# Kernel tuning notes

Hardware: AMD Instinct MI355X
Metric: run time of the kernel (lower is better)

The kernel has to match this reference:

```python
import jax, jax.numpy as jnp
import numpy as np

N_NODES = 100000
N_EDGES = 800000
N_LABEL = 262144
IN, H, OUT = 16, 256, 128
BN_EPS = 1e-5


def setup_inputs() -> dict:
    key = jax.random.key(0)
    ks = jax.random.split(key, 32)
    def lin(k, fi, fo):
        return jax.random.normal(k, (fi, fo), jnp.float32) / np.sqrt(fi)
    inp = {
        "x": jax.random.normal(ks[0], (N_NODES, IN), jnp.float32),
        "edge_index": jax.random.randint(ks[1], (2, N_EDGES), 0, N_NODES, jnp.int32),
        "edge_weight": jax.random.uniform(ks[2], (N_EDGES,), jnp.float32),
        "edge_label_index": jax.random.randint(ks[3], (2, N_LABEL), 0, N_NODES, jnp.int32),
        # encoder GCN layers: 4 convs, BN on first 3
        "W1": lin(ks[4], IN, H),  "b1": jnp.zeros((H,), jnp.float32),
        "g1": jnp.ones((H,), jnp.float32), "be1": jnp.zeros((H,), jnp.float32),
        "W2": lin(ks[5], H, H),   "b2": jnp.zeros((H,), jnp.float32),
        "g2": jnp.ones((H,), jnp.float32), "be2": jnp.zeros((H,), jnp.float32),
        "W3": lin(ks[6], H, H),   "b3": jnp.zeros((H,), jnp.float32),
        "g3": jnp.ones((H,), jnp.float32), "be3": jnp.zeros((H,), jnp.float32),
        "W4": lin(ks[7], H, OUT), "b4": jnp.zeros((OUT,), jnp.float32),
        # decoder MLP on concatenated pair embeddings
        "D1W": lin(ks[8], 2 * OUT, OUT), "D1b": jnp.zeros((OUT,), jnp.float32),
        "D2W": lin(ks[9], OUT, OUT),     "D2b": jnp.zeros((OUT,), jnp.float32),
        "D3W": lin(ks[10], OUT, 1),      "D3b": jnp.zeros((1,), jnp.float32),
    }
    return inp


def _forward(x, edge_index, edge_weight, edge_label_index,
             W1, b1, g1, be1, W2, b2, g2, be2, W3, b3, g3, be3, W4, b4,
             D1W, D1b, D2W, D2b, D3W, D3b):
    n = x.shape[0]
    src, dst = edge_index[0], edge_index[1]
    # GCN symmetric normalization with self-loops (weight 1)
    deg = jax.ops.segment_sum(edge_weight, dst, num_segments=n) + 1.0
    dinv = jax.lax.rsqrt(deg)
    edge_norm = dinv[src] * edge_weight * dinv[dst]   # [E]
    self_norm = dinv * dinv                            # [N]

    def gcn(h, W, b):
        h = h @ W                                      # [N, F]
        agg = jax.ops.segment_sum(h[src] * edge_norm[:, None], dst, num_segments=n)
        return agg + h * self_norm[:, None] + b

    def bn(h, g, be):  # training-mode BatchNorm1d over node dim
        m = h.mean(axis=0)
        v = h.var(axis=0)
        return (h - m) * jax.lax.rsqrt(v + BN_EPS) * g + be

    h = jax.nn.relu(bn(gcn(x, W1, b1), g1, be1))
    h = jax.nn.relu(bn(gcn(h, W2, b2), g2, be2))
    h = jax.nn.relu(bn(gcn(h, W3, b3), g3, be3))
    z = gcn(h, W4, b4)                                 # [N, OUT] encoded

    # decode: gather both endpoints, concat, MLP + sigmoid
    e0, e1 = edge_label_index[0], edge_label_index[1]
    q = jnp.concatenate([z[e0], z[e1]], axis=1)        # [EL, 2*OUT]
    q = jax.nn.relu(q @ D1W + D1b)
    q = jax.nn.relu(q @ D2W + D2b)
    p = jax.nn.sigmoid(q @ D3W + D3b)
    return p.squeeze(-1)                               # [EL]


def reference(x, edge_index, edge_weight, edge_label_index,
              W1, b1, g1, be1, W2, b2, g2, be2, W3, b3, g3, be3, W4, b4,
              D1W, D1b, D2W, D2b, D3W, D3b):
    return _forward(x, edge_index, edge_weight, edge_label_index,
                    W1, b1, g1, be1, W2, b2, g2, be2, W3, b3, g3, be3, W4, b4,
                    D1W, D1b, D2W, D2b, D3W, D3b)
```

## Files before the change

### kernel.cpp

```cpp
#include <hip/hip_runtime.h>
#include <cmath>

#define NN 100000
#define NE 800000
#define NL 262144
#define GB 782

typedef __attribute__((ext_vector_type(8))) short bf16x8;
typedef __attribute__((ext_vector_type(4))) float f32x4;

__device__ __forceinline__ unsigned short f2bf(float f) {
  unsigned int u = __builtin_bit_cast(unsigned int, f);
  u = (u + 0x7FFF + ((u >> 16) & 1)) >> 16;
  return (unsigned short)u;
}
__device__ __forceinline__ float bf2f(unsigned short u) {
  return __builtin_bit_cast(float, (unsigned int)u << 16);
}

__global__ void k_degcnt(const int* __restrict__ dst, const float* __restrict__ w,
                         unsigned long long* __restrict__ dc) {
  int e = blockIdx.x * 256 + threadIdx.x;
  if (e < NE) {
    unsigned long long pk = (1ULL << 32) | (unsigned long long)(unsigned int)(w[e] * 8388608.0f);
    atomicAdd(&dc[dst[e]], pk);
  }
}
__global__ void k_dinv2(const unsigned long long* __restrict__ dc,
                        float* __restrict__ dinv, int* __restrict__ cnt) {
  int n = blockIdx.x * 256 + threadIdx.x;
  if (n < NN) {
    unsigned long long v = dc[n];
    cnt[n] = (int)(v >> 32);
    dinv[n] = rsqrtf((float)(unsigned int)v * (1.0f / 8388608.0f) + 1.0f);
  }
}
__global__ void k_scan1(const int* __restrict__ cnt, int* __restrict__ tsum) {
  __shared__ int s[256];
  int t = threadIdx.x;
  int base = blockIdx.x * 1024;
  int acc = 0;
  for (int i = 0; i < 4; i++) { int idx = base + t * 4 + i; if (idx < NN) acc += cnt[idx]; }
  s[t] = acc; __syncthreads();
  for (int o = 128; o > 0; o >>= 1) { if (t < o) s[t] += s[t + o]; __syncthreads(); }
  if (t == 0) tsum[blockIdx.x] = s[0];
}
__global__ void k_scan2(const int* __restrict__ tsum, int* __restrict__ toff, int nt, int* __restrict__ rowptr_end) {
  __shared__ int s[256];
  int t = threadIdx.x;
  int v = (t < nt) ? tsum[t] : 0;
  s[t] = v; __syncthreads();
  for (int o = 1; o < 256; o <<= 1) { int xv = (t >= o) ? s[t - o] : 0; __syncthreads(); s[t] += xv; __syncthreads(); }
  if (t < nt) toff[t] = s[t] - v;
  if (t == 255) *rowptr_end = s[255];
}
__global__ void k_scan3(const int* __restrict__ cnt, const int* __restrict__ toff,
                        int* __restrict__ rowptr, int* __restrict__ nxt) {
  __shared__ int s[256];
  int t = threadIdx.x;
  int base = blockIdx.x * 1024 + t * 4;
  int v[4]; int tot = 0;
  for (int i = 0; i < 4; i++) { int idx = base + i; v[i] = (idx < NN) ? cnt[idx] : 0; tot += v[i]; }
  s[t] = tot; __syncthreads();
  for (int o = 1; o < 256; o <<= 1) { int xv = (t >= o) ? s[t - o] : 0; __syncthreads(); s[t] += xv; __syncthreads(); }
  int excl = s[t] - tot + toff[blockIdx.x];
  for (int i = 0; i < 4; i++) {
    int idx = base + i;
    if (idx < NN) { rowptr[idx] = excl; nxt[idx] = excl; }
    excl += v[i];
  }
}
__global__ void k_scatter2(const int* __restrict__ src, const int* __restrict__ dst, const float* __restrict__ w,
                           const float* __restrict__ dinv, int* __restrict__ nxt,
                           int* __restrict__ esp, float* __restrict__ enp) {
  int e = blockIdx.x * 256 + threadIdx.x;
  if (e < NE) {
    int d = dst[e], s = src[e];
    int p = atomicAdd(&nxt[d], 1);
    esp[p] = s; enp[p] = dinv[s] * w[e] * dinv[d];
  }
}

__global__ void k_cvt_wT(const float* __restrict__ W, unsigned short* __restrict__ Wt, int K, int N) {
  int id = blockIdx.x * 256 + threadIdx.x;
  if (id >= K * N) return;
  int n = id / K, k = id - n * K;
  Wt[id] = f2bf(W[k * N + n]);
}

__global__ void k_pack(const unsigned short* __restrict__ Wt, unsigned short* __restrict__ P, int K, int NJ) {
  int id = blockIdx.x * 256 + threadIdx.x;
  int total = (K / 32) * NJ * 64;
  if (id >= total) return;
  int lane = id & 63, g = id >> 6;
  int j = g % NJ, s = g / NJ;
  int fr = lane & 15, fq = lane >> 4;
  uint4 v = *(const uint4*)(Wt + (size_t)(j * 16 + fr) * K + s * 32 + fq * 8);
  *(uint4*)(P + (size_t)id * 8) = v;
}

__global__ __launch_bounds__(256) void k_wuv(const float* __restrict__ W4, const float* __restrict__ D1W,
                                             const float* __restrict__ b4, const float* __restrict__ D1b,
                                             unsigned short* __restrict__ wtUV, float* __restrict__ buv) {
  __shared__ float dc[256];
  int j = blockIdx.x;
  int k = threadIdx.x;
  dc[k] = D1W[k * 128 + j];
  __syncthreads();
  float su = 0.f, sv = 0.f;
  const float* w4r = W4 + k * 128;
  for (int p = 0; p < 128; p++) { float w = w4r[p]; su += w * dc[p]; sv += w * dc[128 + p]; }
  wtUV[(size_t)j * 256 + k] = f2bf(su);
  wtUV[(size_t)(128 + j) * 256 + k] = f2bf(sv);
  if (k == 0) {
    float bu = D1b[j], bv = 0.f;
    for (int p = 0; p < 128; p++) { bu += b4[p] * dc[p]; bv += b4[p] * dc[128 + p]; }
    buv[j] = bu; buv[128 + j] = bv;
  }
}

__global__ __launch_bounds__(256) void k_gemm16(const float* __restrict__ x, const float* __restrict__ W,
                                                unsigned short* __restrict__ out) {
  __shared__ float xs[32][16];
  int t = threadIdx.x; int row0 = blockIdx.x * 32;
  for (int i = t; i < 512; i += 256) {
    int r = i >> 4, c = i & 15; int row = row0 + r;
    xs[r][c] = (row < NN) ? x[(size_t)row * 16 + c] : 0.f;
  }
  float w[16];
  #pragma unroll
  for (int k = 0; k < 16; k++) w[k] = W[k * 256 + t];
  __syncthreads();
  for (int r = 0; r < 32; r++) {
    int row = row0 + r; if (row >= NN) break;
    float acc = 0.f;
    #pragma unroll
    for (int k = 0; k < 16; k++) acc += xs[r][k] * w[k];
    out[(size_t)row * 256 + t] = f2bf(acc);
  }
}

template <bool STATS>
__global__ __launch_bounds__(512) void k_gemm_v12(
    const unsigned short* __restrict__ A, const unsigned short* __restrict__ Wp,
    const float* __restrict__ bias, unsigned short* __restrict__ C,
    float* __restrict__ Ps, float* __restrict__ Pq) {
  __shared__ unsigned short S[128 * 264];
  const int t = threadIdx.x;
  const int lane = t & 63, w = t >> 6, fr = lane & 15, fq = lane >> 4;
  const int row0 = blockIdx.x * 128;
  bf16x8 B0[8], B1[8];
  #pragma unroll
  for (int s = 0; s < 8; s++) {
    B0[s] = *(const bf16x8*)(Wp + ((size_t)(s * 16 + 2 * w) * 64 + lane) * 8);
    B1[s] = *(const bf16x8*)(Wp + ((size_t)(s * 16 + 2 * w + 1) * 64 + lane) * 8);
  }
  {
    int r = t >> 2, q = t & 3;
    int row = row0 + r;
    uint4* dst = (uint4*)(S + r * 264 + q * 64);
    if (row < NN) {
      const uint4* src = (const uint4*)(A + (size_t)row * 256 + q * 64);
      #pragma unroll
      for (int i = 0; i < 8; i++) dst[i] = src[i];
    } else {
      #pragma unroll
      for (int i = 0; i < 8; i++) dst[i] = make_uint4(0, 0, 0, 0);
    }
  }
  __syncthreads();
  f32x4 acc[8][2] = {};
  #pragma unroll
  for (int r = 0; r < 8; r++) {
    #pragma unroll
    for (int s = 0; s < 8; s++) {
      bf16x8 a = *(const bf16x8*)(S + (r * 16 + fr) * 264 + s * 32 + fq * 8);
      acc[r][0] = __builtin_amdgcn_mfma_f32_16x16x32_bf16(a, B0[s], acc[r][0], 0, 0, 0);
      acc[r][1] = __builtin_amdgcn_mfma_f32_16x16x32_bf16(a, B1[s], acc[r][1], 0, 0, 0);
    }
  }
  #pragma unroll
  for (int jl = 0; jl < 2; jl++) {
    const int col = w * 32 + jl * 16 + fr;
    float bj = bias[col];
    float s_ = 0.f, q_ = 0.f;
    #pragma unroll
    for (int r = 0; r < 8; r++) {
      #pragma unroll
      for (int rr = 0; rr < 4; rr++) {
        int row = row0 + r * 16 + fq * 4 + rr;
        if (row < NN) {
          float c = acc[r][jl][rr] + bj;
          C[(size_t)row * 256 + col] = f2bf(c);
          if (STATS) { s_ += c; q_ += c * c; }
        }
      }
    }
    if (STATS) {
      s_ += __shfl_xor(s_, 16); q_ += __shfl_xor(q_, 16);
      s_ += __shfl_xor(s_, 32); q_ += __shfl_xor(q_, 32);
      if (fq == 0) {
        Ps[(size_t)blockIdx.x * 256 + col] = s_;
        Pq[(size_t)blockIdx.x * 256 + col] = q_;
      }
    }
  }
}

__global__ __launch_bounds__(256) void k_bnred(const float* __restrict__ Ps, const float* __restrict__ Pq,
                                               const float* __restrict__ g, const float* __restrict__ be,
                                               float* __restrict__ scale, float* __restrict__ shift) {
  __shared__ float Ss[256], Sq[256];
  const int f = blockIdx.x;
  const int t = threadIdx.x;
  float s = 0.f, q = 0.f;
  for (int p = t; p < GB; p += 256) { s += Ps[(size_t)p * 256 + f]; q += Pq[(size_t)p * 256 + f]; }
  Ss[t] = s; Sq[t] = q;
  __syncthreads();
  for (int o = 128; o > 0; o >>= 1) { if (t < o) { Ss[t] += Ss[t + o]; Sq[t] += Sq[t + o]; } __syncthreads(); }
  if (t == 0) {
    float m = Ss[0] * (1.f / NN);
    float v = Sq[0] * (1.f / NN) - m * m;
    float sc = g[f] * rsqrtf(v + 1e-5f);
    scale[f] = sc; shift[f] = be[f] - m * sc;
  }
}

__device__ __forceinline__ void ld8(const unsigned short* p, float* f) {
  uint4 v = *(const uint4*)p;
  unsigned int u[4] = {v.x, v.y, v.z, v.w};
  #pragma unroll
  for (int i = 0; i < 4; i++) {
    f[2 * i] = bf2f((unsigned short)(u[i] & 0xFFFF));
    f[2 * i + 1] = bf2f((unsigned short)(u[i] >> 16));
  }
}
template <bool BN>
__global__ __launch_bounds__(256) void k_agg5(const unsigned short* __restrict__ hb,
    const int* __restrict__ esp, const float* __restrict__ enp,
    const int* __restrict__ rowptr, const float* __restrict__ dinv,
    const float* __restrict__ scale, const float* __restrict__ shift,
    const float* __restrict__ bias, unsigned short* __restrict__ outb) {
  const int lane = threadIdx.x & 63;
  const int lg = lane & 31;
  const int srcbase = lane & 32;
  const int n = blockIdx.x * 8 + (threadIdx.x >> 5);
  const int f0 = lg * 8;
  float sc8[8] = {}, sh8[8] = {};
  if constexpr (BN) {
    #pragma unroll
    for (int j = 0; j < 8; j++) { sc8[j] = scale[f0 + j]; sh8[j] = shift[f0 + j]; }
  }
  auto xf = [&](float v, int j) -> float {
    if constexpr (BN) return fmaxf(v * sc8[j] + sh8[j], 0.f);
    else return v;
  };
  float d = dinv[n]; float dd = d * d;
  float acc[8];
  {
    float sv[8];
    ld8(hb + (size_t)n * 256 + f0, sv);
    #pragma unroll
    for (int j = 0; j < 8; j++) acc[j] = xf(sv[j], j) * dd + (BN ? 0.f : bias[f0 + j]);
  }
  const int i0 = rowptr[n];
  const int dg = rowptr[n + 1] - i0;
  int sreg = 0; float wreg = 0.f;
  if (lg < dg) { sreg = esp[i0 + lg]; wreg = enp[i0 + lg]; }
  const int m = (dg < 32) ? dg : 32;
  int e = 0;
  for (; e + 4 <= m; e += 4) {
    int s0 = __shfl(sreg, srcbase | e), s1 = __shfl(sreg, srcbase | (e + 1));
    int s2 = __shfl(sreg, srcbase | (e + 2)), s3 = __shfl(sreg, srcbase | (e + 3));
    float w0 = __shfl(wreg, srcbase | e), w1 = __shfl(wreg, srcbase | (e + 1));
    float w2 = __shfl(wreg, srcbase | (e + 2)), w3 = __shfl(wreg, srcbase | (e + 3));
    float r0[8], r1[8], r2[8], r3[8];
    ld8(hb + (size_t)s0 * 256 + f0, r0);
    ld8(hb + (size_t)s1 * 256 + f0, r1);
    ld8(hb + (size_t)s2 * 256 + f0, r2);
    ld8(hb + (size_t)s3 * 256 + f0, r3);
    #pragma unroll
    for (int j = 0; j < 8; j++)
      acc[j] += w0 * xf(r0[j], j) + w1 * xf(r1[j], j) + w2 * xf(r2[j], j) + w3 * xf(r3[j], j);
  }
  for (; e < m; e++) {
    int s0 = __shfl(sreg, srcbase | e); float w0 = __shfl(wreg, srcbase | e);
    float r0[8];
    ld8(hb + (size_t)s0 * 256 + f0, r0);
    #pragma unroll
    for (int j = 0; j < 8; j++) acc[j] += w0 * xf(r0[j], j);
  }
  for (int i = i0 + 32; i < i0 + dg; i++) {
    int s0 = esp[i]; float w0 = enp[i];
    float r0[8];
    ld8(hb + (size_t)s0 * 256 + f0, r0);
    #pragma unroll
    for (int j = 0; j < 8; j++) acc[j] += w0 * xf(r0[j], j);
  }
  unsigned int o[4];
  #pragma unroll
  for (int i = 0; i < 4; i++)
    o[i] = (unsigned int)f2bf(acc[2 * i]) | ((unsigned int)f2bf(acc[2 * i + 1]) << 16);
  *(uint4*)(outb + (size_t)n * 256 + f0) = make_uint4(o[0], o[1], o[2], o[3]);
}

__global__ __launch_bounds__(256) void k_bnstats2(const unsigned short* __restrict__ h,
                                                  float* __restrict__ sums, float* __restrict__ sqs) {
  __shared__ float L[4][256];
  int t = threadIdx.x;
  int fp = t & 127;
  size_t rbase = (size_t)blockIdx.x * 256 + (t >> 7);
  float s0 = 0, q0 = 0, s1 = 0, q1 = 0;
  for (int i = 0; i < 128; i++) {
    size_t r = rbase + 2 * (size_t)i;
    if (r >= NN) break;
    unsigned int v = *(const unsigned int*)&h[r * 256 + fp * 2];
    float a = bf2f((unsigned short)(v & 0xFFFF));
    float b = bf2f((unsigned short)(v >> 16));
    s0 += a; q0 += a * a; s1 += b; q1 += b * b;
  }
  L[0][t] = s0; L[1][t] = q0; L[2][t] = s1; L[3][t] = q1;
  __syncthreads();
  if (t < 128) {
    s0 = L[0][t] + L[0][t + 128]; q0 = L[1][t] + L[1][t + 128];
    s1 = L[2][t] + L[2][t + 128]; q1 = L[3][t] + L[3][t + 128];
    atomicAdd(&sums[2 * t], s0); atomicAdd(&sqs[2 * t], q0);
    atomicAdd(&sums[2 * t + 1], s1); atomicAdd(&sqs[2 * t + 1], q1);
  }
}
__global__ void k_bnfinal(const float* __restrict__ sums, const float* __restrict__ sqs,
                          const float* __restrict__ g, const float* __restrict__ be,
                          float* __restrict__ scale, float* __restrict__ shift) {
  int f = threadIdx.x;
  float m = sums[f] * (1.f / NN);
  float v = sqs[f] * (1.f / NN) - m * m;
  float sc = g[f] * rsqrtf(v + 1e-5f);
  scale[f] = sc; shift[f] = be[f] - m * sc;
}

__global__ __launch_bounds__(256) void k_decoder3(
    const unsigned short* __restrict__ uv,
    const int* __restrict__ l0, const int* __restrict__ l1,
    const unsigned short* __restrict__ W2p, const float* __restrict__ D2b,
    const float* __restrict__ D3W, const float* __restrict__ D3b,
    float* __restrict__ out) {
  __shared__ unsigned short S[128 * 136];
  __shared__ int ei0[128], ei1[128];
  const int t = threadIdx.x;
  const int base = blockIdx.x * 128;
  if (t < 128) ei0[t] = l0[base + t];
  else ei1[t - 128] = l1[base + t - 128];
  __syncthreads();
  {
    int e = t >> 1, h = t & 1;
    const uint4* pu = (const uint4*)(uv + (size_t)ei0[e] * 256 + h * 64);
    const uint4* pv = (const uint4*)(uv + (size_t)ei1[e] * 256 + 128 + h * 64);
    uint4* dst = (uint4*)(S + e * 136 + h * 64);
    #pragma unroll
    for (int i = 0; i < 8; i++) {
      uint4 a = pu[i], b = pv[i];
      unsigned int ia[4] = {a.x, a.y, a.z, a.w};
      unsigned int ib[4] = {b.x, b.y, b.z, b.w};
      unsigned int o[4];
      #pragma unroll
      for (int p = 0; p < 4; p++) {
        float lo = fmaxf(bf2f((unsigned short)(ia[p] & 0xFFFF)) + bf2f((unsigned short)(ib[p] & 0xFFFF)), 0.f);
        float hi = fmaxf(bf2f((unsigned short)(ia[p] >> 16)) + bf2f((unsigned short)(ib[p] >> 16)), 0.f);
        o[p] = (unsigned int)f2bf(lo) | ((unsigned int)f2bf(hi) << 16);
      }
      dst[i] = make_uint4(o[0], o[1], o[2], o[3]);
    }
  }
  __syncthreads();
  const int lane = t & 63, w = t >> 6, fr = lane & 15, fq = lane >> 4;
  f32x4 acc2[2][8] = {};
  #pragma unroll
  for (int s = 0; s < 4; s++) {
    bf16x8 a0 = *(const bf16x8*)(S + (w * 32 + fr) * 136 + s * 32 + fq * 8);
    bf16x8 a1 = *(const bf16x8*)(S + (w * 32 + 16 + fr) * 136 + s * 32 + fq * 8);
    #pragma unroll
    for (int j = 0; j < 8; j++) {
      bf16x8 bw = *(const bf16x8*)(W2p + ((size_t)(s * 8 + j) * 64 + lane) * 8);
      acc2[0][j] = __builtin_amdgcn_mfma_f32_16x16x32_bf16(a0, bw, acc2[0][j], 0, 0, 0);
      acc2[1][j] = __builtin_amdgcn_mfma_f32_16x16x32_bf16(a1, bw, acc2[1][j], 0, 0, 0);
    }
  }
  float b2v[8], w3v[8];
  #pragma unroll
  for (int j = 0; j < 8; j++) { b2v[j] = D2b[j * 16 + fr]; w3v[j] = D3W[j * 16 + fr]; }
  float d3b = D3b[0];
  #pragma unroll
  for (int f = 0; f < 2; f++) {
    float p[4] = {0.f, 0.f, 0.f, 0.f};
    #pragma unroll
    for (int j = 0; j < 8; j++)
      #pragma unroll
      for (int r = 0; r < 4; r++)
        p[r] += fmaxf(acc2[f][j][r] + b2v[j], 0.f) * w3v[j];
    #pragma unroll
    for (int r = 0; r < 4; r++) {
      p[r] += __shfl_xor(p[r], 1);
      p[r] += __shfl_xor(p[r], 2);
      p[r] += __shfl_xor(p[r], 4);
      p[r] += __shfl_xor(p[r], 8);
      if (fr == 0) out[base + w * 32 + f * 16 + fq * 4 + r] = 1.f / (1.f + expf(-(p[r] + d3b)));
    }
  }
}

extern "C" void kernel_launch(void* const* d_in, const int* in_sizes, int n_in,
                              void* d_out, int out_size, void* d_ws, size_t ws_size,
                              hipStream_t stream) {
  const float* x = (const float*)d_in[0];
  const int* ei = (const int*)d_in[1];
  const int* esrc = ei; const int* edst = ei + NE;
  const float* ew = (const float*)d_in[2];
  const int* eli = (const int*)d_in[3];
  const int* l0 = eli; const int* l1 = eli + NL;
  const float* W1 = (const float*)d_in[4],  *b1 = (const float*)d_in[5];
  const float* g1 = (const float*)d_in[6],  *be1 = (const float*)d_in[7];
  const float* W2 = (const float*)d_in[8],  *b2 = (const float*)d_in[9];
  const float* g2 = (const float*)d_in[10], *be2 = (const float*)d_in[11];
  const float* W3 = (const float*)d_in[12], *b3 = (const float*)d_in[13];
  const float* g3 = (const float*)d_in[14], *be3 = (const float*)d_in[15];
  const float* W4 = (const float*)d_in[16], *b4 = (const float*)d_in[17];
  const float* D1W = (const float*)d_in[18], *D1b = (const float*)d_in[19];
  const float* D2W = (const float*)d_in[20], *D2b = (const float*)d_in[21];
  const float* D3W = (const float*)d_in[22], *D3b = (const float*)d_in[23];
  float* out = (float*)d_out;

  float* wf = (float*)d_ws;
  size_t off = 0;
  auto A = [&](size_t n) { float* p = wf + off; off += (n + 63) & ~(size_t)63; return p; };
  float* dinv = A(NN);
  float* enp = A(NE);
  float* sums = A(256);
  float* sqs = A(256);
  float* scale = A(256);
  float* shift = A(256);
  float* buv = A(256);
  float* Ps = A((size_t)GB * 256);
  float* Pq = A((size_t)GB * 256);
  unsigned long long* dc = (unsigned long long*)A(2 * (size_t)NN);
  int* cnt = (int*)A(NN);
  int* rowptr = (int*)A(NN + 1);
  int* nxt = (int*)A(NN);
  int* esp = (int*)A(NE);
  int* tsum = (int*)A(256);
  int* toff = (int*)A(256);
  unsigned short* hbA = (unsigned short*)A((size_t)NN * 128);
  unsigned short* hbB = (unsigned short*)A((size_t)NN * 128);
  unsigned short* uv  = (unsigned short*)A((size_t)NN * 128);
  unsigned short* wt2 = (unsigned short*)A(256 * 128);
  unsigned short* wt3 = (unsigned short*)A(256 * 128);
  unsigned short* wtUV = (unsigned short*)A(256 * 128);
  unsigned short* w2t = (unsigned short*)A(64 * 128);
  unsigned short* wp2 = (unsigned short*)A(256 * 128);
  unsigned short* wp3 = (unsigned short*)A(256 * 128);
  unsigned short* wpUV = (unsigned short*)A(256 * 128);
  unsigned short* w2p = (unsigned short*)A(64 * 128);

  const int EB = (NE + 255) / 256;
  const int NB = (NN + 255) / 256;
  const int ST = (NN + 1023) / 1024;
  const int AB = NN / 8;

  hipMemsetAsync(dc, 0, (size_t)NN * 8, stream);
  k_degcnt<<<EB, 256, 0, stream>>>(edst, ew, dc);
  k_dinv2<<<NB, 256, 0, stream>>>(dc, dinv, cnt);
  k_scan1<<<ST, 256, 0, stream>>>(cnt, tsum);
  k_scan2<<<1, 256, 0, stream>>>(tsum, toff, ST, rowptr + NN);
  k_scan3<<<ST, 256, 0, stream>>>(cnt, toff, rowptr, nxt);
  k_scatter2<<<EB, 256, 0, stream>>>(esrc, edst, ew, dinv, nxt, esp, enp);

  k_cvt_wT<<<(256 * 256 + 255) / 256, 256, 0, stream>>>(W2, wt2, 256, 256);
  k_cvt_wT<<<(256 * 256 + 255) / 256, 256, 0, stream>>>(W3, wt3, 256, 256);
  k_cvt_wT<<<(128 * 128 + 255) / 256, 256, 0, stream>>>(D2W, w2t, 128, 128);
  k_wuv<<<128, 256, 0, stream>>>(W4, D1W, b4, D1b, wtUV, buv);
  k_pack<<<32, 256, 0, stream>>>(wt2, wp2, 256, 16);
  k_pack<<<32, 256, 0, stream>>>(wt3, wp3, 256, 16);
  k_pack<<<32, 256, 0, stream>>>(wtUV, wpUV, 256, 16);
  k_pack<<<8, 256, 0, stream>>>(w2t, w2p, 128, 8);

  k_gemm16<<<(NN + 31) / 32, 256, 0, stream>>>(x, W1, hbA);
  k_agg5<false><<<AB, 256, 0, stream>>>(hbA, esp, enp, rowptr, dinv, nullptr, nullptr, b1, hbB);
  hipMemsetAsync(sums, 0, 512 * sizeof(float), stream);
  k_bnstats2<<<NB, 256, 0, stream>>>(hbB, sums, sqs);
  k_bnfinal<<<1, 256, 0, stream>>>(sums, sqs, g1, be1, scale, shift);

  k_agg5<true><<<AB, 256, 0, stream>>>(hbB, esp, enp, rowptr, dinv, scale, shift, nullptr, hbA);
  k_gemm_v12<true><<<GB, 512, 0, stream>>>(hbA, wp2, b2, hbB, Ps, Pq);
  k_bnred<<<256, 256, 0, stream>>>(Ps, Pq, g2, be2, scale, shift);

  k_agg5<true><<<AB, 256, 0, stream>>>(hbB, esp, enp, rowptr, dinv, scale, shift, nullptr, hbA);
  k_gemm_v12<true><<<GB, 512, 0, stream>>>(hbA, wp3, b3, hbB, Ps, Pq);
  k_bnred<<<256, 256, 0, stream>>>(Ps, Pq, g3, be3, scale, shift);

  k_agg5<true><<<AB, 256, 0, stream>>>(hbB, esp, enp, rowptr, dinv, scale, shift, nullptr, hbA);
  k_gemm_v12<false><<<GB, 512, 0, stream>>>(hbA, wpUV, buv, uv, nullptr, nullptr);

  k_decoder3<<<NL / 128, 256, 0, stream>>>(uv, l0, l1, w2p, D2b, D3W, D3b, out);
}
```

Baseline: 708.5 us.

## Reorder aggregation and matmul to aggregate on narrow feature widths

Layer 1 now aggregates the raw 16-wide input features before the 16x256 matmul. BN statistics are computed in the GEMM epilogue, which replaces the separate stats and final kernels. Layer 4 now applies BN+ReLU while loading the GEMM input, multiplies by W4 to 128 columns, aggregates at width 128, and then applies D1 as a separate 128->256 GEMM, instead of the folded W4·D1 256-wide product aggregated at 256. The goal is to cut gather traffic in the edge aggregations at the cost of one extra GEMM pass and an extra intermediate write and read in layer 4.

Result: faster. 606.9 us (-14.3%).

```diff
diff --git a/kernel.cpp b/kernel.cpp
--- a/kernel.cpp
+++ b/kernel.cpp
@@ -5,6 +5,7 @@
 #define NE 800000
 #define NL 262144
 #define GB 782
+#define NP1 3125
 
 typedef __attribute__((ext_vector_type(8))) short bf16x8;
 typedef __attribute__((ext_vector_type(4))) float f32x4;
@@ -87,6 +88,17 @@
   int n = id / K, k = id - n * K;
   Wt[id] = f2bf(W[k * N + n]);
 }
+__global__ void k_cvt_d1(const float* __restrict__ D1W, unsigned short* __restrict__ Wt) {
+  int id = blockIdx.x * 256 + threadIdx.x;
+  if (id >= 256 * 128) return;
+  int n = id >> 7, k = id & 127;
+  float v = (n < 128) ? D1W[(size_t)k * 128 + n] : D1W[(size_t)(128 + k) * 128 + (n - 128)];
+  Wt[id] = f2bf(v);
+}
+__global__ void k_biasuv(const float* __restrict__ D1b, float* __restrict__ buv) {
+  int t = threadIdx.x;
+  buv[t] = (t < 128) ? D1b[t] : 0.f;
+}
 
 __global__ void k_pack(const unsigned short* __restrict__ Wt, unsigned short* __restrict__ P, int K, int NJ) {
   int id = blockIdx.x * 256 + threadIdx.x;
@@ -99,89 +111,152 @@
   *(uint4*)(P + (size_t)id * 8) = v;
 }
 
-__global__ __launch_bounds__(256) void k_wuv(const float* __restrict__ W4, const float* __restrict__ D1W,
-                                             const float* __restrict__ b4, const float* __restrict__ D1b,
-                                             unsigned short* __restrict__ wtUV, float* __restrict__ buv) {
-  __shared__ float dc[256];
-  int j = blockIdx.x;
-  int k = threadIdx.x;
-  dc[k] = D1W[k * 128 + j];
-  __syncthreads();
-  float su = 0.f, sv = 0.f;
-  const float* w4r = W4 + k * 128;
-  for (int p = 0; p < 128; p++) { float w = w4r[p]; su += w * dc[p]; sv += w * dc[128 + p]; }
-  wtUV[(size_t)j * 256 + k] = f2bf(su);
-  wtUV[(size_t)(128 + j) * 256 + k] = f2bf(sv);
-  if (k == 0) {
-    float bu = D1b[j], bv = 0.f;
-    for (int p = 0; p < 128; p++) { bu += b4[p] * dc[p]; bv += b4[p] * dc[128 + p]; }
-    buv[j] = bu; buv[128 + j] = bv;
-  }
-}
-
-__global__ __launch_bounds__(256) void k_gemm16(const float* __restrict__ x, const float* __restrict__ W,
-                                                unsigned short* __restrict__ out) {
-  __shared__ float xs[32][16];
+__global__ __launch_bounds__(256) void k_agg16(const float* __restrict__ x,
+    const int* __restrict__ esp, const float* __restrict__ enp,
+    const int* __restrict__ rowptr, const float* __restrict__ dinv,
+    float* __restrict__ ax) {
+  const int t = threadIdx.x;
+  const int lane = t & 63;
+  const int g = lane >> 2, gl = lane & 3;
+  const int n = blockIdx.x * 64 + (t >> 6) * 16 + g;
+  if (n >= NN) return;
+  const float4* x4 = (const float4*)x;
+  float d = dinv[n]; float dd = d * d;
+  float4 self = x4[(size_t)n * 4 + gl];
+  float4 acc = make_float4(self.x * dd, self.y * dd, self.z * dd, self.w * dd);
+  const int i0 = rowptr[n];
+  const int dg = rowptr[n + 1] - i0;
+  int sreg[4]; float wreg[4];
+  #pragma unroll
+  for (int k = 0; k < 4; k++) {
+    int idx = gl + 4 * k;
+    if (idx < dg) { sreg[k] = esp[i0 + idx]; wreg[k] = enp[i0 + idx]; }
+    else { sreg[k] = 0; wreg[k] = 0.f; }
+  }
+  const int gbase = lane & ~3;
+  const int m4 = ((dg < 16 ? dg : 16) + 3) & ~3;
+  #pragma unroll 4
+  for (int e = 0; e < m4; e += 4) {
+    int k = e >> 2;
+    int s0, s1, s2, s3; float w0, w1, w2, w3;
+    switch (k) {
+      case 0: s0=__shfl(sreg[0],gbase|0); s1=__shfl(sreg[0],gbase|1); s2=__shfl(sreg[0],gbase|2); s3=__shfl(sreg[0],gbase|3);
+              w0=__shfl(wreg[0],gbase|0); w1=__shfl(wreg[0],gbase|1); w2=__shfl(wreg[0],gbase|2); w3=__shfl(wreg[0],gbase|3); break;
+      case 1: s0=__shfl(sreg[1],gbase|0); s1=__shfl(sreg[1],gbase|1); s2=__shfl(sreg[1],gbase|2); s3=__shfl(sreg[1],gbase|3);
+              w0=__shfl(wreg[1],gbase|0); w1=__shfl(wreg[1],gbase|1); w2=__shfl(wreg[1],gbase|2); w3=__shfl(wreg[1],gbase|3); break;
+      case 2: s0=__shfl(sreg[2],gbase|0); s1=__shfl(sreg[2],gbase|1); s2=__shfl(sreg[2],gbase|2); s3=__shfl(sreg[2],gbase|3);
+              w0=__shfl(wreg[2],gbase|0); w1=__shfl(wreg[2],gbase|1); w2=__shfl(wreg[2],gbase|2); w3=__shfl(wreg[2],gbase|3); break;
+      default: s0=__shfl(sreg[3],gbase|0); s1=__shfl(sreg[3],gbase|1); s2=__shfl(sreg[3],gbase|2); s3=__shfl(sreg[3],gbase|3);
+              w0=__shfl(wreg[3],gbase|0); w1=__shfl(wreg[3],gbase|1); w2=__shfl(wreg[3],gbase|2); w3=__shfl(wreg[3],gbase|3); break;
+    }
+    float4 r0 = x4[(size_t)s0 * 4 + gl], r1 = x4[(size_t)s1 * 4 + gl];
+    float4 r2 = x4[(size_t)s2 * 4 + gl], r3 = x4[(size_t)s3 * 4 + gl];
+    acc.x += w0 * r0.x + w1 * r1.x + w2 * r2.x + w3 * r3.x;
+    acc.y += w0 * r0.y + w1 * r1.y + w2 * r2.y + w3 * r3.y;
+    acc.z += w0 * r0.z + w1 * r1.z + w2 * r2.z + w3 * r3.z;
+    acc.w += w0 * r0.w + w1 * r1.w + w2 * r2.w + w3 * r3.w;
+  }
+  for (int i = i0 + 16; i < i0 + dg; i++) {
+    int s0 = esp[i]; float w0 = enp[i];
+    float4 r0 = x4[(size_t)s0 * 4 + gl];
+    acc.x += w0 * r0.x; acc.y += w0 * r0.y; acc.z += w0 * r0.z; acc.w += w0 * r0.w;
+  }
+  ((float4*)ax)[(size_t)n * 4 + gl] = acc;
+}
+
+__global__ __launch_bounds__(256) void k_gemm16s(const float* __restrict__ ax, const float* __restrict__ W,
+                                                 const float* __restrict__ b, unsigned short* __restrict__ out,
+                                                 float* __restrict__ Ps, float* __restrict__ Pq) {
+  __shared__ float xs[32][17];
   int t = threadIdx.x; int row0 = blockIdx.x * 32;
   for (int i = t; i < 512; i += 256) {
     int r = i >> 4, c = i & 15; int row = row0 + r;
-    xs[r][c] = (row < NN) ? x[(size_t)row * 16 + c] : 0.f;
+    xs[r][c] = (row < NN) ? ax[(size_t)row * 16 + c] : 0.f;
   }
   float w[16];
   #pragma unroll
   for (int k = 0; k < 16; k++) w[k] = W[k * 256 + t];
+  float bt = b[t];
   __syncthreads();
+  float s_ = 0.f, q_ = 0.f;
   for (int r = 0; r < 32; r++) {
     int row = row0 + r; if (row >= NN) break;
-    float acc = 0.f;
+    float acc = bt;
     #pragma unroll
     for (int k = 0; k < 16; k++) acc += xs[r][k] * w[k];
     out[(size_t)row * 256 + t] = f2bf(acc);
-  }
-}
-
-template <bool STATS>
+    s_ += acc; q_ += acc * acc;
+  }
+  Ps[(size_t)blockIdx.x * 256 + t] = s_;
+  Pq[(size_t)blockIdx.x * 256 + t] = q_;
+}
+
+template <int KDIM, int NCOLS, bool STATS, bool BNA>
 __global__ __launch_bounds__(512) void k_gemm_v12(
     const unsigned short* __restrict__ A, const unsigned short* __restrict__ Wp,
-    const float* __restrict__ bias, unsigned short* __restrict__ C,
-    float* __restrict__ Ps, float* __restrict__ Pq) {
-  __shared__ unsigned short S[128 * 264];
+    const float* __restrict__ bias, const float* __restrict__ bnsc, const float* __restrict__ bnsh,
+    unsigned short* __restrict__ C, float* __restrict__ Ps, float* __restrict__ Pq) {
+  constexpr int CPW = NCOLS / 128;
+  constexpr int KS = KDIM / 32;
+  constexpr int LDA = KDIM + 8;
+  constexpr int NU4 = KDIM / 32;
+  __shared__ unsigned short S[128 * LDA];
+  __shared__ float sc[BNA ? KDIM : 1], sh[BNA ? KDIM : 1];
   const int t = threadIdx.x;
   const int lane = t & 63, w = t >> 6, fr = lane & 15, fq = lane >> 4;
   const int row0 = blockIdx.x * 128;
-  bf16x8 B0[8], B1[8];
-  #pragma unroll
-  for (int s = 0; s < 8; s++) {
-    B0[s] = *(const bf16x8*)(Wp + ((size_t)(s * 16 + 2 * w) * 64 + lane) * 8);
-    B1[s] = *(const bf16x8*)(Wp + ((size_t)(s * 16 + 2 * w + 1) * 64 + lane) * 8);
-  }
+  if (BNA) {
+    if (t < KDIM) { sc[t] = bnsc[t]; sh[t] = bnsh[t]; }
+    __syncthreads();
+  }
+  bf16x8 B[CPW][KS];
+  #pragma unroll
+  for (int c = 0; c < CPW; c++)
+    #pragma unroll
+    for (int s = 0; s < KS; s++)
+      B[c][s] = *(const bf16x8*)(Wp + ((size_t)(s * (NCOLS / 16) + (w * CPW + c)) * 64 + lane) * 8);
   {
     int r = t >> 2, q = t & 3;
     int row = row0 + r;
-    uint4* dst = (uint4*)(S + r * 264 + q * 64);
+    uint4* dst = (uint4*)(S + r * LDA + q * (KDIM / 4));
     if (row < NN) {
-      const uint4* src = (const uint4*)(A + (size_t)row * 256 + q * 64);
+      const uint4* src = (const uint4*)(A + (size_t)row * KDIM + q * (KDIM / 4));
       #pragma unroll
-      for (int i = 0; i < 8; i++) dst[i] = src[i];
+      for (int i = 0; i < NU4; i++) {
+        uint4 v = src[i];
+        if (BNA) {
+          unsigned int u[4] = {v.x, v.y, v.z, v.w};
+          #pragma unroll
+          for (int p = 0; p < 4; p++) {
+            int colb = q * (KDIM / 4) + i * 8 + p * 2;
+            float lo = fmaxf(bf2f((unsigned short)(u[p] & 0xFFFF)) * sc[colb] + sh[colb], 0.f);
+            float hi = fmaxf(bf2f((unsigned short)(u[p] >> 16)) * sc[colb + 1] + sh[colb + 1], 0.f);
+            u[p] = (unsigned int)f2bf(lo) | ((unsigned int)f2bf(hi) << 16);
+          }
+          v = make_uint4(u[0], u[1], u[2], u[3]);
+        }
+        dst[i] = v;
+      }
     } else {
       #pragma unroll
-      for (int i = 0; i < 8; i++) dst[i] = make_uint4(0, 0, 0, 0);
+      for (int i = 0; i < NU4; i++) dst[i] = make_uint4(0, 0, 0, 0);
     }
   }
   __syncthreads();
-  f32x4 acc[8][2] = {};
+  f32x4 acc[8][CPW] = {};
   #pragma unroll
   for (int r = 0; r < 8; r++) {
     #pragma unroll
-    for (int s = 0; s < 8; s++) {
-      bf16x8 a = *(const bf16x8*)(S + (r * 16 + fr) * 264 + s * 32 + fq * 8);
-      acc[r][0] = __builtin_amdgcn_mfma_f32_16x16x32_bf16(a, B0[s], acc[r][0], 0, 0, 0);
-      acc[r][1] = __builtin_amdgcn_mfma_f32_16x16x32_bf16(a, B1[s], acc[r][1], 0, 0, 0);
-    }
-  }
-  #pragma unroll
-  for (int jl = 0; jl < 2; jl++) {
-    const int col = w * 32 + jl * 16 + fr;
+    for (int s = 0; s < KS; s++) {
+      bf16x8 a = *(const bf16x8*)(S + (r * 16 + fr) * LDA + s * 32 + fq * 8);
+      #pragma unroll
+      for (int c = 0; c < CPW; c++)
+        acc[r][c] = __builtin_amdgcn_mfma_f32_16x16x32_bf16(a, B[c][s], acc[r][c], 0, 0, 0);
+    }
+  }
+  #pragma unroll
+  for (int c = 0; c < CPW; c++) {
+    const int col = w * (16 * CPW) + c * 16 + fr;
     float bj = bias[col];
     float s_ = 0.f, q_ = 0.f;
     #pragma unroll
@@ -190,9 +265,9 @@
       for (int rr = 0; rr < 4; rr++) {
         int row = row0 + r * 16 + fq * 4 + rr;
         if (row < NN) {
-          float c = acc[r][jl][rr] + bj;
-          C[(size_t)row * 256 + col] = f2bf(c);
-          if (STATS) { s_ += c; q_ += c * c; }
+          float cv = acc[r][c][rr] + bj;
+          C[(size_t)row * NCOLS + col] = f2bf(cv);
+          if (STATS) { s_ += cv; q_ += cv * cv; }
         }
       }
     }
@@ -209,12 +284,12 @@
 
 __global__ __launch_bounds__(256) void k_bnred(const float* __restrict__ Ps, const float* __restrict__ Pq,
                                                const float* __restrict__ g, const float* __restrict__ be,
-                                               float* __restrict__ scale, float* __restrict__ shift) {
+                                               float* __restrict__ scale, float* __restrict__ shift, int np) {
   __shared__ float Ss[256], Sq[256];
   const int f = blockIdx.x;
   const int t = threadIdx.x;
   float s = 0.f, q = 0.f;
-  for (int p = t; p < GB; p += 256) { s += Ps[(size_t)p * 256 + f]; q += Pq[(size_t)p * 256 + f]; }
+  for (int p = t; p < np; p += 256) { s += Ps[(size_t)p * 256 + f]; q += Pq[(size_t)p * 256 + f]; }
   Ss[t] = s; Sq[t] = q;
   __syncthreads();
   for (int o = 128; o > 0; o >>= 1) { if (t < o) { Ss[t] += Ss[t + o]; Sq[t] += Sq[t + o]; } __syncthreads(); }
@@ -226,42 +301,49 @@
   }
 }
 
-__device__ __forceinline__ void ld8(const unsigned short* p, float* f) {
-  uint4 v = *(const uint4*)p;
-  unsigned int u[4] = {v.x, v.y, v.z, v.w};
-  #pragma unroll
-  for (int i = 0; i < 4; i++) {
-    f[2 * i] = bf2f((unsigned short)(u[i] & 0xFFFF));
-    f[2 * i + 1] = bf2f((unsigned short)(u[i] >> 16));
-  }
-}
-template <bool BN>
+template <int FPL>
+__device__ __forceinline__ void ldF(const unsigned short* p, float* f) {
+  if constexpr (FPL == 8) {
+    uint4 v = *(const uint4*)p;
+    unsigned int u[4] = {v.x, v.y, v.z, v.w};
+    #pragma unroll
+    for (int i = 0; i < 4; i++) {
+      f[2 * i] = bf2f((unsigned short)(u[i] & 0xFFFF));
+      f[2 * i + 1] = bf2f((unsigned short)(u[i] >> 16));
+    }
+  } else {
+    ushort4 v = *(const ushort4*)p;
+    f[0] = bf2f(v.x); f[1] = bf2f(v.y); f[2] = bf2f(v.z); f[3] = bf2f(v.w);
+  }
+}
+template <bool BN, int F>
 __global__ __launch_bounds__(256) void k_agg5(const unsigned short* __restrict__ hb,
     const int* __restrict__ esp, const float* __restrict__ enp,
     const int* __restrict__ rowptr, const float* __restrict__ dinv,
     const float* __restrict__ scale, const float* __restrict__ shift,
     const float* __restrict__ bias, unsigned short* __restrict__ outb) {
+  constexpr int FPL = F / 32;
   const int lane = threadIdx.x & 63;
   const int lg = lane & 31;
   const int srcbase = lane & 32;
   const int n = blockIdx.x * 8 + (threadIdx.x >> 5);
-  const int f0 = lg * 8;
-  float sc8[8] = {}, sh8[8] = {};
+  const int f0 = lg * FPL;
+  float sc8[FPL] = {}, sh8[FPL] = {};
   if constexpr (BN) {
     #pragma unroll
-    for (int j = 0; j < 8; j++) { sc8[j] = scale[f0 + j]; sh8[j] = shift[f0 + j]; }
+    for (int j = 0; j < FPL; j++) { sc8[j] = scale[f0 + j]; sh8[j] = shift[f0 + j]; }
   }
   auto xf = [&](float v, int j) -> float {
     if constexpr (BN) return fmaxf(v * sc8[j] + sh8[j], 0.f);
     else return v;
   };
   float d = dinv[n]; float dd = d * d;
-  float acc[8];
+  float acc[FPL];
   {
-    float sv[8];
-    ld8(hb + (size_t)n * 256 + f0, sv);
-    #pragma unroll
-    for (int j = 0; j < 8; j++) acc[j] = xf(sv[j], j) * dd + (BN ? 0.f : bias[f0 + j]);
+    float sv[FPL];
+    ldF<FPL>(hb + (size_t)n * F + f0, sv);
+    #pragma unroll
+    for (int j = 0; j < FPL; j++) acc[j] = xf(sv[j], j) * dd + (BN ? 0.f : bias[f0 + j]);
   }
   const int i0 = rowptr[n];
   const int dg = rowptr[n + 1] - i0;
@@ -274,68 +356,39 @@
     int s2 = __shfl(sreg, srcbase | (e + 2)), s3 = __shfl(sreg, srcbase | (e + 3));
     float w0 = __shfl(wreg, srcbase | e), w1 = __shfl(wreg, srcbase | (e + 1));
     float w2 = __shfl(wreg, srcbase | (e + 2)), w3 = __shfl(wreg, srcbase | (e + 3));
-    float r0[8], r1[8], r2[8], r3[8];
-    ld8(hb + (size_t)s0 * 256 + f0, r0);
-    ld8(hb + (size_t)s1 * 256 + f0, r1);
-    ld8(hb + (size_t)s2 * 256 + f0, r2);
-    ld8(hb + (size_t)s3 * 256 + f0, r3);
-    #pragma unroll
-    for (int j = 0; j < 8; j++)
+    float r0[FPL], r1[FPL], r2[FPL], r3[FPL];
+    ldF<FPL>(hb + (size_t)s0 * F + f0, r0);
+    ldF<FPL>(hb + (size_t)s1 * F + f0, r1);
+    ldF<FPL>(hb + (size_t)s2 * F + f0, r2);
+    ldF<FPL>(hb + (size_t)s3 * F + f0, r3);
+    #pragma unroll
+    for (int j = 0; j < FPL; j++)
       acc[j] += w0 * xf(r0[j], j) + w1 * xf(r1[j], j) + w2 * xf(r2[j], j) + w3 * xf(r3[j], j);
   }
   for (; e < m; e++) {
     int s0 = __shfl(sreg, srcbase | e); float w0 = __shfl(wreg, srcbase | e);
-    float r0[8];
-    ld8(hb + (size_t)s0 * 256 + f0, r0);
-    #pragma unroll
-    for (int j = 0; j < 8; j++) acc[j] += w0 * xf(r0[j], j);
+    float r0[FPL];
+    ldF<FPL>(hb + (size_t)s0 * F + f0, r0);
+    #pragma unroll
+    for (int j = 0; j < FPL; j++) acc[j] += w0 * xf(r0[j], j);
   }
   for (int i = i0 + 32; i < i0 + dg; i++) {
     int s0 = esp[i]; float w0 = enp[i];
-    float r0[8];
-    ld8(hb + (size_t)s0 * 256 + f0, r0);
-    #pragma unroll
-    for (int j = 0; j < 8; j++) acc[j] += w0 * xf(r0[j], j);
-  }
-  unsigned int o[4];
-  #pragma unroll
-  for (int i = 0; i < 4; i++)
-    o[i] = (unsigned int)f2bf(acc[2 * i]) | ((unsigned int)f2bf(acc[2 * i + 1]) << 16);
-  *(uint4*)(outb + (size_t)n * 256 + f0) = make_uint4(o[0], o[1], o[2], o[3]);
-}
-
-__global__ __launch_bounds__(256) void k_bnstats2(const unsigned short* __restrict__ h,
-                                                  float* __restrict__ sums, float* __restrict__ sqs) {
-  __shared__ float L[4][256];
-  int t = threadIdx.x;
-  int fp = t & 127;
-  size_t rbase = (size_t)blockIdx.x * 256 + (t >> 7);
-  float s0 = 0, q0 = 0, s1 = 0, q1 = 0;
-  for (int i = 0; i < 128; i++) {
-    size_t r = rbase + 2 * (size_t)i;
-    if (r >= NN) break;
-    unsigned int v = *(const unsigned int*)&h[r * 256 + fp * 2];
-    float a = bf2f((unsigned short)(v & 0xFFFF));
-    float b = bf2f((unsigned short)(v >> 16));
-    s0 += a; q0 += a * a; s1 += b; q1 += b * b;
-  }
-  L[0][t] = s0; L[1][t] = q0; L[2][t] = s1; L[3][t] = q1;
-  __syncthreads();
-  if (t < 128) {
-    s0 = L[0][t] + L[0][t + 128]; q0 = L[1][t] + L[1][t + 128];
-    s1 = L[2][t] + L[2][t + 128]; q1 = L[3][t] + L[3][t + 128];
-    atomicAdd(&sums[2 * t], s0); atomicAdd(&sqs[2 * t], q0);
-    atomicAdd(&sums[2 * t + 1], s1); atomicAdd(&sqs[2 * t + 1], q1);
-  }
-}
-__global__ void k_bnfinal(const float* __restrict__ sums, const float* __restrict__ sqs,
-                          const float* __restrict__ g, const float* __restrict__ be,
-                          float* __restrict__ scale, float* __restrict__ shift) {
-  int f = threadIdx.x;
-  float m = sums[f] * (1.f / NN);
-  float v = sqs[f] * (1.f / NN) - m * m;
-  float sc = g[f] * rsqrtf(v + 1e-5f);
-  scale[f] = sc; shift[f] = be[f] - m * sc;
+    float r0[FPL];
+    ldF<FPL>(hb + (size_t)s0 * F + f0, r0);
+    #pragma unroll
+    for (int j = 0; j < FPL; j++) acc[j] += w0 * xf(r0[j], j);
+  }
+  if constexpr (FPL == 8) {
+    unsigned int o[4];
+    #pragma unroll
+    for (int i = 0; i < 4; i++)
+      o[i] = (unsigned int)f2bf(acc[2 * i]) | ((unsigned int)f2bf(acc[2 * i + 1]) << 16);
+    *(uint4*)(outb + (size_t)n * F + f0) = make_uint4(o[0], o[1], o[2], o[3]);
+  } else {
+    ushort4 o; o.x = f2bf(acc[0]); o.y = f2bf(acc[1]); o.z = f2bf(acc[2]); o.w = f2bf(acc[3]);
+    *(ushort4*)(outb + (size_t)n * F + f0) = o;
+  }
 }
 
 __global__ __launch_bounds__(256) void k_decoder3(
@@ -434,13 +487,13 @@
   auto A = [&](size_t n) { float* p = wf + off; off += (n + 63) & ~(size_t)63; return p; };
   float* dinv = A(NN);
   float* enp = A(NE);
-  float* sums = A(256);
-  float* sqs = A(256);
   float* scale = A(256);
   float* shift = A(256);
   float* buv = A(256);
-  float* Ps = A((size_t)GB * 256);
-  float* Pq = A((size_t)GB * 256);
+  float* zero128 = A(128);
+  float* Ps = A((size_t)NP1 * 256);
+  float* Pq = A((size_t)NP1 * 256);
+  float* axf = A((size_t)NN * 16);
   unsigned long long* dc = (unsigned long long*)A(2 * (size_t)NN);
   int* cnt = (int*)A(NN);
   int* rowptr = (int*)A(NN + 1);
@@ -453,19 +506,23 @@
   unsigned short* uv  = (unsigned short*)A((size_t)NN * 128);
   unsigned short* wt2 = (unsigned short*)A(256 * 128);
   unsigned short* wt3 = (unsigned short*)A(256 * 128);
-  unsigned short* wtUV = (unsigned short*)A(256 * 128);
+  unsigned short* wt4 = (unsigned short*)A(128 * 128);
+  unsigned short* wtD1 = (unsigned short*)A(128 * 128);
   unsigned short* w2t = (unsigned short*)A(64 * 128);
   unsigned short* wp2 = (unsigned short*)A(256 * 128);
   unsigned short* wp3 = (unsigned short*)A(256 * 128);
-  unsigned short* wpUV = (unsigned short*)A(256 * 128);
+  unsigned short* wp4 = (unsigned short*)A(128 * 128);
+  unsigned short* wpD1 = (unsigned short*)A(128 * 128);
   unsigned short* w2p = (unsigned short*)A(64 * 128);
 
   const int EB = (NE + 255) / 256;
   const int NB = (NN + 255) / 256;
   const int ST = (NN + 1023) / 1024;
   const int AB = NN / 8;
+  const int AG16 = (NN + 63) / 64;
 
   hipMemsetAsync(dc, 0, (size_t)NN * 8, stream);
+  hipMemsetAsync(zero128, 0, 128 * sizeof(float), stream);
   k_degcnt<<<EB, 256, 0, stream>>>(edst, ew, dc);
   k_dinv2<<<NB, 256, 0, stream>>>(dc, dinv, cnt);
   k_scan1<<<ST, 256, 0, stream>>>(cnt, tsum);
@@ -475,29 +532,31 @@
 
   k_cvt_wT<<<(256 * 256 + 255) / 256, 256, 0, stream>>>(W2, wt2, 256, 256);
   k_cvt_wT<<<(256 * 256 + 255) / 256, 256, 0, stream>>>(W3, wt3, 256, 256);
+  k_cvt_wT<<<(256 * 128 + 255) / 256, 256, 0, stream>>>(W4, wt4, 256, 128);
+  k_cvt_d1<<<(256 * 128 + 255) / 256, 256, 0, stream>>>(D1W, wtD1);
   k_cvt_wT<<<(128 * 128 + 255) / 256, 256, 0, stream>>>(D2W, w2t, 128, 128);
-  k_wuv<<<128, 256, 0, stream>>>(W4, D1W, b4, D1b, wtUV, buv);
+  k_biasuv<<<1, 256, 0, stream>>>(D1b, buv);
   k_pack<<<32, 256, 0, stream>>>(wt2, wp2, 256, 16);
   k_pack<<<32, 256, 0, stream>>>(wt3, wp3, 256, 16);
-  k_pack<<<32, 256, 0, stream>>>(wtUV, wpUV, 256, 16);
+  k_pack<<<16, 256, 0, stream>>>(wt4, wp4, 256, 8);
+  k_pack<<<16, 256, 0, stream>>>(wtD1, wpD1, 128, 16);
   k_pack<<<8, 256, 0, stream>>>(w2t, w2p, 128, 8);
 
-  k_gemm16<<<(NN + 31) / 32, 256, 0, stream>>>(x, W1, hbA);
-  k_agg5<false><<<AB, 256, 0, stream>>>(hbA, esp, enp, rowptr, dinv, nullptr, nullptr, b1, hbB);
-  hipMemsetAsync(sums, 0, 512 * sizeof(float), stream);
-  k_bnstats2<<<NB, 256, 0, stream>>>(hbB, sums, sqs);
-  k_bnfinal<<<1, 256, 0, stream>>>(sums, sqs, g1, be1, scale, shift);
-
-  k_agg5<true><<<AB, 256, 0, stream>>>(hbB, esp, enp, rowptr, dinv, scale, shift, nullptr, hbA);
-  k_gemm_v12<true><<<GB, 512, 0, stream>>>(hbA, wp2, b2, hbB, Ps, Pq);
-  k_bnred<<<256, 256, 0, stream>>>(Ps, Pq, g2, be2, scale, shift);
-
-  k_agg5<true><<<AB, 256, 0, stream>>>(hbB, esp, enp, rowptr, dinv, scale, shift, nullptr, hbA);
-  k_gemm_v12<true><<<GB, 512, 0, stream>>>(hbA, wp3, b3, hbB, Ps, Pq);
-  k_bnred<<<256, 256, 0, stream>>>(Ps, Pq, g3, be3, scale, shift);
-
-  k_agg5<true><<<AB, 256, 0, stream>>>(hbB, esp, enp, rowptr, dinv, scale, shift, nullptr, hbA);
-  k_gemm_v12<false><<<GB, 512, 0, stream>>>(hbA, wpUV, buv, uv, nullptr, nullptr);
+  k_agg16<<<AG16, 256, 0, stream>>>(x, esp, enp, rowptr, dinv, axf);
+  k_gemm16s<<<NP1, 256, 0, stream>>>(axf, W1, b1, hbB, Ps, Pq);
+  k_bnred<<<256, 256, 0, stream>>>(Ps, Pq, g1, be1, scale, shift, NP1);
+
+  k_agg5<true, 256><<<AB, 256, 0, stream>>>(hbB, esp, enp, rowptr, dinv, scale, shift, nullptr, hbA);
+  k_gemm_v12<256, 256, true, false><<<GB, 512, 0, stream>>>(hbA, wp2, b2, nullptr, nullptr, hbB, Ps, Pq);
+  k_bnred<<<256, 256, 0, stream>>>(Ps, Pq, g2, be2, scale, shift, GB);
+
+  k_agg5<true, 256><<<AB, 256, 0, stream>>>(hbB, esp, enp, rowptr, dinv, scale, shift, nullptr, hbA);
+  k_gemm_v12<256, 256, true, false><<<GB, 512, 0, stream>>>(hbA, wp3, b3, nullptr, nullptr, hbB, Ps, Pq);
+  k_bnred<<<256, 256, 0, stream>>>(Ps, Pq, g3, be3, scale, shift, GB);
+
+  k_gemm_v12<256, 128, false, true><<<GB, 512, 0, stream>>>(hbB, wp4, zero128, scale, shift, hbA, nullptr, nullptr);
+  k_agg5<false, 128><<<AB, 256, 0, stream>>>(hbA, esp, enp, rowptr, dinv, nullptr, nullptr, b4, hbB);
+  k_gemm_v12<128, 256, false, false><<<GB, 512, 0, stream>>>(hbB, wpD1, buv, nullptr, nullptr, uv, nullptr, nullptr);
 
   k_decoder3<<<NL / 128, 256, 0, stream>>>(uv, l0, l1, w2p, D2b, D3W, D3b, out);
 }
```
